# Performance work log

Hardware: AMD Instinct MI355X
Metric: run time of the kernel (lower is better)

## Reference

```python
import jax, jax.numpy as jnp
import numpy as np

EPS = 1e-5

def _layer_norm_last(x):
    # F.layer_norm over the last dim, no affine
    m = jnp.mean(x, axis=-1, keepdims=True)
    v = jnp.var(x, axis=-1, keepdims=True)
    return (x - m) * jax.lax.rsqrt(v + EPS)

def setup_inputs() -> dict:
    key = jax.random.key(0)
    ks = jax.random.split(key, 4)
    N, C, H, W = 8, 512, 32, 32
    G = 8
    x = jax.random.normal(ks[0], (N, C, H, W), dtype=jnp.float32)
    w_qkv = jax.random.normal(ks[1], (3 * C, C), dtype=jnp.float32) * 0.02
    relative = jax.random.normal(ks[2], (3, 2 * C - 1), dtype=jnp.float32)
    bn_w = jnp.ones((3 * G,), dtype=jnp.float32)
    bn_b = jnp.zeros((3 * G,), dtype=jnp.float32)
    return {
        "x": x, "w_qkv": w_qkv, "relative": relative,
        "bn_w": bn_w, "bn_b": bn_b,
        "f_qr": jnp.float32(0.1), "f_kr": jnp.float32(0.1),
        "f_sv": jnp.float32(1.0), "f_sve": jnp.float32(0.1),
        "gamma": jnp.full((1,), 0.5, dtype=jnp.float32),
    }

def reference(x, w_qkv, relative, bn_w, bn_b, f_qr, f_kr, f_sv, f_sve, gamma):
    N, C, H, W = x.shape
    HW = H * W
    G = bn_w.shape[0] // 3          # groups
    gp = HW // G                    # group_planes

    # qkv transform (1x1 conv == matmul over channels) + layernorm over spatial
    x1 = x.reshape(N, C, HW)
    x1 = jnp.einsum('oc,bci->boi', w_qkv, x1)          # (N, 3C, HW)
    x1 = _layer_norm_last(x1)

    qkv = x1.reshape(N, G, 3 * C, gp)                  # row-major, matches torch
    q = qkv[:, :, :C]                                  # (N, G, C, gp)
    k = qkv[:, :, C:2 * C]
    v = qkv[:, :, 2 * C:]

    # relative position embeddings gathered to (3, C, C)
    qi = jnp.arange(C)[None, :]
    ki = jnp.arange(C)[:, None]
    rel_idx = (ki - qi + C - 1).reshape(-1)            # (C*C,) int
    emb = relative[:, rel_idx].reshape(3, C, C)
    qE, kE, vE = emb[0], emb[1], emb[2]

    # 'bgci,icj->bgcj' with emb repeated along i collapses to sum over i then outer
    qr = jnp.einsum('bgci,cj->bgcj', q, qE) * f_qr     # (N, G, C, C)
    kr = jnp.swapaxes(jnp.einsum('bgci,cj->bgcj', k, kE), 2, 3) * f_kr
    qk = jnp.einsum('bgci,bgji->bgcj', q, k)           # (N, G, C, C)

    ss = jnp.concatenate([qk, qr, kr], axis=1)         # (N, 3G, C, C)
    # BatchNorm2d (training mode: batch stats over N, C, C axes)
    mu = jnp.mean(ss, axis=(0, 2, 3), keepdims=True)
    var = jnp.var(ss, axis=(0, 2, 3), keepdims=True)
    ss = (ss - mu) * jax.lax.rsqrt(var + EPS)
    ss = ss * bn_w.reshape(1, -1, 1, 1) + bn_b.reshape(1, -1, 1, 1)

    ss = ss.reshape(N, 3, G, C, C).sum(axis=1)         # (N, G, C, C)
    sim = jax.nn.softmax(ss, axis=3)

    sv = jnp.einsum('bgci,bgij->bgjc', sim, v) * f_sv  # (N, G, gp, C)
    # 'bgci,jci->bgjc' with vE repeated along j -> same value for every j
    sve = jnp.einsum('bgci,ci->bgc', sim, vE) * f_sve  # (N, G, C)
    sve = jnp.broadcast_to(sve[:, :, None, :], sv.shape)

    so = jnp.concatenate([sv, sve], axis=-1).reshape(N, HW * 2, C)
    so = jnp.swapaxes(_layer_norm_last(jnp.swapaxes(so, 1, 2)), 1, 2)
    out = so.reshape(N, G, gp, 2, C).sum(axis=-2).reshape(N, C, H, W)
    return gamma.reshape(()) * out + x
```

## Files before the change

kernel.cpp:

```cpp
#include <hip/hip_runtime.h>
#include <math.h>

#define DEV_INLINE __device__ __forceinline__

typedef short bf16x8 __attribute__((ext_vector_type(8)));
typedef float f32x4  __attribute__((ext_vector_type(4)));


DEV_INLINE float bf2f(short h){
  union { unsigned u; float f; } x; x.u = ((unsigned)(unsigned short)h) << 16; return x.f;
}
DEV_INLINE short f2bf(float f){
  union { float f; unsigned u; } x; x.f = f;
  unsigned r = x.u + 0x7FFF + ((x.u >> 16) & 1);
  return (short)(r >> 16);
}

template<bool MAXOP>
DEV_INLINE float block_reduce_f(float v){
  __shared__ float tmp[4];
  const int lane = threadIdx.x & 63, w = threadIdx.x >> 6;
  #pragma unroll
  for (int off = 32; off; off >>= 1){
    float o = __shfl_down(v, off);
    v = MAXOP ? fmaxf(v, o) : (v + o);
  }
  __syncthreads();
  if (lane == 0) tmp[w] = v;
  __syncthreads();
  return MAXOP ? fmaxf(fmaxf(tmp[0], tmp[1]), fmaxf(tmp[2], tmp[3]))
               : (tmp[0] + tmp[1] + tmp[2] + tmp[3]);
}

DEV_INLINE double block_reduce_d(double v){
  __shared__ double tmp[4];
  const int lane = threadIdx.x & 63, w = threadIdx.x >> 6;
  #pragma unroll
  for (int off = 32; off; off >>= 1) v += __shfl_down(v, off);
  __syncthreads();
  if (lane == 0) tmp[w] = v;
  __syncthreads();
  return tmp[0] + tmp[1] + tmp[2] + tmp[3];
}


DEV_INLINE void stage_tile(const short* __restrict__ g, int ldk, char* lds_region, int t){
  #pragma unroll
  for (int r = 0; r < 2; ++r){
    int o   = t * 16 + r * 4096;
    int row = o >> 6, wb = o & 63;
    int swb = wb ^ (((row >> 1) & 3) << 4);
    const short* src = g + (size_t)row * ldk + (swb >> 1);
    char* dst = lds_region + ((t >> 6) << 10) + (r << 12);
    __builtin_amdgcn_global_load_lds((const __attribute__((address_space(1))) void*)src,
                                     (__attribute__((address_space(3))) void*)dst, 16, 0, 0);
  }
}

DEV_INLINE bf16x8 read_frag(const char* base, int row, int kgrp){
  int off = row * 64 + ((kgrp ^ ((row >> 1) & 3)) << 4);
  return *(const bf16x8*)(base + off);
}

template<int KTILES>
DEV_INLINE void mfma_loop(const short* __restrict__ A, int ldA,
                          const short* __restrict__ B, int ldB,
                          char* ldsA, char* ldsB, int t, f32x4 acc[4][4]){
  const int l = t & 63, w = t >> 6;
  const int wr = (w >> 1) * 64, wc = (w & 1) * 64;
  for (int kt = 0; kt < KTILES; ++kt){
    stage_tile(A + kt * 32, ldA, ldsA, t);
    stage_tile(B + kt * 32, ldB, ldsB, t);
    __syncthreads();
    bf16x8 af[4], bfr[4];
    #pragma unroll
    for (int m = 0; m < 4; ++m) af[m]  = read_frag(ldsA, wr + m * 16 + (l & 15), l >> 4);
    #pragma unroll
    for (int n = 0; n < 4; ++n) bfr[n] = read_frag(ldsB, wc + n * 16 + (l & 15), l >> 4);
    #pragma unroll
    for (int m = 0; m < 4; ++m)
      #pragma unroll
      for (int n = 0; n < 4; ++n)
        acc[m][n] = __builtin_amdgcn_mfma_f32_16x16x32_bf16(af[m], bfr[n], acc[m][n], 0, 0, 0);
    __syncthreads();
  }
}

__global__ __launch_bounds__(256) void k_cvtW(const float* __restrict__ W, short* __restrict__ Wbf,
                                              double* __restrict__ stats, float* __restrict__ S12){
  const int gi = blockIdx.x * 256 + threadIdx.x;
  if (gi < 48) stats[gi] = 0.0;
  if (gi < 8192) S12[gi] = 0.f;
  int i = gi * 4;
  float4 v = *(const float4*)(W + i);
  short4 o; o.x = f2bf(v.x); o.y = f2bf(v.y); o.z = f2bf(v.z); o.w = f2bf(v.w);
  *(short4*)(Wbf + i) = o;
}

__global__ __launch_bounds__(256) void k_cvtXt(const float* __restrict__ X, short* __restrict__ Xt){
  const int b = blockIdx.z, kt = blockIdx.y, it = blockIdx.x;
  __shared__ short s[64][72];
  const int t = threadIdx.x;
  const int rl = t >> 2, cs = (t & 3) * 16;
  const float* src = X + ((size_t)b * 512 + kt * 64 + rl) * 1024 + it * 64 + cs;
  #pragma unroll
  for (int e = 0; e < 16; e += 4){
    float4 v = *(const float4*)(src + e);
    s[rl][cs + e + 0] = f2bf(v.x); s[rl][cs + e + 1] = f2bf(v.y);
    s[rl][cs + e + 2] = f2bf(v.z); s[rl][cs + e + 3] = f2bf(v.w);
  }
  __syncthreads();
  bf16x8 a0, a1;
  #pragma unroll
  for (int e = 0; e < 8; ++e){ a0[e] = s[cs + e][rl]; a1[e] = s[cs + 8 + e][rl]; }
  short* dst = Xt + ((size_t)b * 1024 + it * 64 + rl) * 512 + kt * 64 + cs;
  *(bf16x8*)dst = a0;
  *(bf16x8*)(dst + 8) = a1;
}

__global__ __launch_bounds__(256) void k_vt(const short* __restrict__ Ybf, short* __restrict__ Vt){
  const int bg = blockIdx.z, iit = blockIdx.y, jt = blockIdx.x;
  const int b = bg >> 3, g = bg & 7;
  const short* V = Ybf + (size_t)(b * 1536 + g * 192 + 128) * 1024;
  __shared__ short s[64][72];
  const int t = threadIdx.x;
  const int rl = t >> 2, cs = (t & 3) * 16;
  const short* src = V + (size_t)(iit * 64 + rl) * 128 + jt * 64 + cs;
  *(bf16x8*)&s[rl][cs]     = *(const bf16x8*)src;
  *(bf16x8*)&s[rl][cs + 8] = *(const bf16x8*)(src + 8);
  __syncthreads();
  bf16x8 a0, a1;
  #pragma unroll
  for (int e = 0; e < 8; ++e){ a0[e] = s[cs + e][rl]; a1[e] = s[cs + 8 + e][rl]; }
  short* dst = Vt + ((size_t)bg * 128 + jt * 64 + rl) * 512 + iit * 64 + cs;
  *(bf16x8*)dst = a0;
  *(bf16x8*)(dst + 8) = a1;
}

__global__ __launch_bounds__(256) void k_gemm1(const short* __restrict__ Wbf,
                                               const short* __restrict__ Xt,
                                               short* __restrict__ Ybf){
  const int b = blockIdx.z, mt = blockIdx.y, nt = blockIdx.x;
  __shared__ char lds[16384];
  const int t = threadIdx.x;
  f32x4 acc[4][4];
  #pragma unroll
  for (int m = 0; m < 4; ++m)
    #pragma unroll
    for (int n = 0; n < 4; ++n) acc[m][n] = {0.f, 0.f, 0.f, 0.f};
  const short* A = Wbf + (size_t)mt * 128 * 512;
  const short* B = Xt + (size_t)b * 1024 * 512 + (size_t)nt * 128 * 512;
  mfma_loop<16>(A, 512, B, 512, lds, lds + 8192, t, acc);
  const int l = t & 63, w = t >> 6, wr = (w >> 1) * 64, wc = (w & 1) * 64;
  short* out = Ybf + (size_t)b * 1536 * 1024 + (size_t)(mt * 128 + wr) * 1024 + nt * 128 + wc;
  #pragma unroll
  for (int m = 0; m < 4; ++m)
    #pragma unroll
    for (int n = 0; n < 4; ++n)
      #pragma unroll
      for (int j = 0; j < 4; ++j)
        out[(size_t)(m * 16 + (l >> 4) * 4 + j) * 1024 + n * 16 + (l & 15)] = f2bf(acc[m][n][j]);
}

__global__ __launch_bounds__(256) void k_ln(short* __restrict__ Ybf,
                                            float* __restrict__ QS, float* __restrict__ KS){
  const int row = blockIdx.x * 4 + (threadIdx.x >> 6);
  const int l = threadIdx.x & 63;
  short* p = Ybf + (size_t)row * 1024 + l * 16;
  bf16x8 v0 = *(const bf16x8*)p;
  bf16x8 v1 = *(const bf16x8*)(p + 8);
  float f[16];
  #pragma unroll
  for (int e = 0; e < 8; ++e){ f[e] = bf2f(v0[e]); f[8 + e] = bf2f(v1[e]); }
  float s1 = 0.f, s2 = 0.f;
  #pragma unroll
  for (int e = 0; e < 16; ++e){ s1 += f[e]; s2 += f[e] * f[e]; }
  #pragma unroll
  for (int off = 32; off; off >>= 1){ s1 += __shfl_xor(s1, off); s2 += __shfl_xor(s2, off); }
  float mean = s1 * (1.f / 1024.f);
  float r = rsqrtf(s2 * (1.f / 1024.f) - mean * mean + 1e-5f);
  float cs = 0.f;
  #pragma unroll
  for (int e = 0; e < 16; ++e){ f[e] = (f[e] - mean) * r; cs += f[e]; }
  bf16x8 o0, o1;
  #pragma unroll
  for (int e = 0; e < 8; ++e){ o0[e] = f2bf(f[e]); o1[e] = f2bf(f[8 + e]); }
  *(bf16x8*)p = o0;
  *(bf16x8*)(p + 8) = o1;
  cs += __shfl_xor(cs, 1); cs += __shfl_xor(cs, 2); cs += __shfl_xor(cs, 4);
  const int o = row % 1536, ol = o % 192;
  if ((l & 7) == 0 && ol < 128){
    const int b = row / 1536, g = o / 192;
    const int c = (ol & 63) * 8 + (l >> 3);
    const int idx = (b * 8 + g) * 512 + c;
    if (ol < 64) QS[idx] = cs; else KS[idx] = cs;
  }
}

__global__ __launch_bounds__(256) void k_rel_rowsums(const float* __restrict__ rel,
                                                     float* __restrict__ R){
  const int c = blockIdx.x * 256 + threadIdx.x;
  float a1 = 0, a2 = 0, b1 = 0, b2 = 0;
  for (int d = 0; d < 512; ++d){
    float v0 = rel[c + d];        a1 += v0; a2 += v0*v0;
    float v1 = rel[1023 + c + d]; b1 += v1; b2 += v1*v1;
  }
  R[c] = a1; R[512 + c] = a2; R[1024 + c] = b1; R[1536 + c] = b2;
}

__global__ __launch_bounds__(256) void k_qk(const short* __restrict__ Ybf,
                                            short* __restrict__ QKbf,
                                            double* __restrict__ stats){
  const int bg = blockIdx.z, mt = blockIdx.y, nt = blockIdx.x;
  const int b = bg >> 3, g = bg & 7;
  __shared__ char lds[16384];
  const int t = threadIdx.x;
  f32x4 acc[4][4];
  #pragma unroll
  for (int m = 0; m < 4; ++m)
    #pragma unroll
    for (int n = 0; n < 4; ++n) acc[m][n] = {0.f, 0.f, 0.f, 0.f};
  const short* q  = Ybf + (size_t)(b * 1536 + g * 192) * 1024;
  const short* kp = q + 65536;
  mfma_loop<4>(q + (size_t)mt * 128 * 128, 128, kp + (size_t)nt * 128 * 128, 128,
               lds, lds + 8192, t, acc);
  const int l = t & 63, w = t >> 6, wr = (w >> 1) * 64, wc = (w & 1) * 64;
  short* out = QKbf + (size_t)bg * 512 * 512 + (size_t)(mt * 128 + wr) * 512 + nt * 128 + wc;
  float s1 = 0.f, s2 = 0.f;
  #pragma unroll
  for (int m = 0; m < 4; ++m)
    #pragma unroll
    for (int n = 0; n < 4; ++n)
      #pragma unroll
      for (int j = 0; j < 4; ++j){
        float vl = acc[m][n][j];
        s1 += vl; s2 += vl * vl;
        out[(size_t)(m * 16 + (l >> 4) * 4 + j) * 512 + n * 16 + (l & 15)] = f2bf(vl);
      }
  float S1 = block_reduce_f<false>(s1);
  float S2 = block_reduce_f<false>(s2);
  if (t == 0){
    atomicAdd(&stats[g * 6 + 0], (double)S1);
    atomicAdd(&stats[g * 6 + 1], (double)S2);
  }
}

__global__ __launch_bounds__(256) void k_qrkr_stats(const float* __restrict__ QS,
                                                    const float* __restrict__ KS,
                                                    const float* __restrict__ R,
                                                    double* __restrict__ stats){
  const int g = blockIdx.x, t = threadIdx.x;
  double sq1 = 0, sq2 = 0, sk1 = 0, sk2 = 0;
  for (int c = t; c < 512; c += 256){
    float qa = 0, qb = 0, ka = 0, kb = 0;
    for (int b = 0; b < 8; ++b){
      float v = QS[(size_t)(b * 8 + g) * 512 + c]; qa += v; qb += v * v;
      float w = KS[(size_t)(b * 8 + g) * 512 + c]; ka += w; kb += w * w;
    }
    sq1 += (double)R[c]        * qa;
    sq2 += (double)R[512 + c]  * qb;
    sk1 += (double)R[1024 + c] * ka;
    sk2 += (double)R[1536 + c] * kb;
  }
  sq1 = block_reduce_d(sq1);
  sq2 = block_reduce_d(sq2);
  sk1 = block_reduce_d(sk1);
  sk2 = block_reduce_d(sk2);
  if (t == 0){
    stats[g * 6 + 2] = sq1; stats[g * 6 + 3] = sq2;
    stats[g * 6 + 4] = sk1; stats[g * 6 + 5] = sk2;
  }
}

__global__ void k_finalize(const double* __restrict__ stats,
                           const float* __restrict__ bnw, const float* __restrict__ bnb,
                           const float* __restrict__ fqr, const float* __restrict__ fkr,
                           float* __restrict__ coefs){
  const int g = threadIdx.x;
  if (g >= 8) return;
  const double M = 2097152.0;
  double mu0  = stats[g*6+0] / M;
  double var0 = stats[g*6+1] / M - mu0*mu0;
  double A0 = (double)bnw[g] / sqrt(var0 + 1e-5);
  double fq = (double)fqr[0];
  double mu1  = fq * stats[g*6+2] / M;
  double var1 = fq*fq * stats[g*6+3] / M - mu1*mu1;
  double A1 = (double)bnw[8+g] / sqrt(var1 + 1e-5);
  double fk = (double)fkr[0];
  double mu2  = fk * stats[g*6+4] / M;
  double var2 = fk*fk * stats[g*6+5] / M - mu2*mu2;
  double A2 = (double)bnw[16+g] / sqrt(var2 + 1e-5);
  double Cg = ((double)bnb[g] - mu0*A0) + ((double)bnb[8+g] - mu1*A1) + ((double)bnb[16+g] - mu2*A2);
  coefs[g*4+0] = (float)A0;
  coefs[g*4+1] = (float)(A1 * fq);
  coefs[g*4+2] = (float)(A2 * fk);
  coefs[g*4+3] = (float)Cg;
}

__global__ __launch_bounds__(256) void k_softmax(short* __restrict__ QKbf,
    const float* __restrict__ QS, const float* __restrict__ KS,
    const float* __restrict__ rel, const float* __restrict__ coefs,
    const float* __restrict__ fsve, float* __restrict__ SVE, float* __restrict__ S12){
  const int row = blockIdx.x * 4 + (threadIdx.x >> 6);
  const int l = threadIdx.x & 63;
  const int bg = row >> 9, c = row & 511, g = bg & 7;
  const float A0 = coefs[g*4+0], B2 = coefs[g*4+2], Cg = coefs[g*4+3];
  const float B1q = coefs[g*4+1] * QS[row];
  short* __restrict__ qkrow = QKbf + (size_t)row * 512;
  const float* __restrict__ ksrow = KS + (size_t)bg * 512;
  const int j0 = l * 8;
  bf16x8 qk8 = *(const bf16x8*)(qkrow + j0);
  float4 ks0 = *(const float4*)(ksrow + j0);
  float4 ks1 = *(const float4*)(ksrow + j0 + 4);
  float ks[8] = {ks0.x, ks0.y, ks0.z, ks0.w, ks1.x, ks1.y, ks1.z, ks1.w};
  const float* relq = rel + 511 + c - j0;
  const float* relk = rel + 1534 + j0 - c;
  float s[8];
  float m = -1e30f;
  #pragma unroll
  for (int e = 0; e < 8; ++e){
    s[e] = A0 * bf2f(qk8[e]) + B1q * relq[-e] + B2 * ks[e] * relk[e] + Cg;
    m = fmaxf(m, s[e]);
  }
  #pragma unroll
  for (int off = 32; off; off >>= 1) m = fmaxf(m, __shfl_xor(m, off));
  float sum = 0.f;
  #pragma unroll
  for (int e = 0; e < 8; ++e){ s[e] = __expf(s[e] - m); sum += s[e]; }
  #pragma unroll
  for (int off = 32; off; off >>= 1) sum += __shfl_xor(sum, off);
  const float inv = 1.0f / sum;
  const float* relv = rel + 2557 + c - j0;
  float sve = 0.f;
  bf16x8 p8;
  #pragma unroll
  for (int e = 0; e < 8; ++e){
    float p = s[e] * inv;
    p8[e] = f2bf(p);
    sve += p * relv[-e];
  }
  *(bf16x8*)(qkrow + j0) = p8;
  #pragma unroll
  for (int off = 32; off; off >>= 1) sve += __shfl_xor(sve, off);
  if (l == 0){
    float e = fsve[0] * sve;
    SVE[row] = e;
    const int b = bg >> 3;
    atomicAdd(&S12[b * 512 + c],        128.f * e);
    atomicAdd(&S12[4096 + b * 512 + c], 128.f * e * e);
  }
}

__global__ __launch_bounds__(256) void k_sv(const short* __restrict__ Pbf,
                                            const short* __restrict__ Vt,
                                            const float* __restrict__ fsv,
                                            short* __restrict__ SV2,
                                            float* __restrict__ S12){
  const int bg = blockIdx.z, mt = blockIdx.x;
  __shared__ char lds[16384];
  __shared__ float s1buf[128], s2buf[128];
  const int t = threadIdx.x;
  s1buf[t & 127] = 0.f; s2buf[t & 127] = 0.f;
  f32x4 acc[4][4];
  #pragma unroll
  for (int m = 0; m < 4; ++m)
    #pragma unroll
    for (int n = 0; n < 4; ++n) acc[m][n] = {0.f, 0.f, 0.f, 0.f};
  const short* A = Pbf + (size_t)bg * 512 * 512 + (size_t)mt * 128 * 512;
  const short* B = Vt  + (size_t)bg * 128 * 512;
  mfma_loop<16>(A, 512, B, 512, lds, lds + 8192, t, acc);
  const int l = t & 63, w = t >> 6, wr = (w >> 1) * 64, wc = (w & 1) * 64;
  const float fv = fsv[0];
  short* out = SV2 + (size_t)bg * 512 * 128 + (size_t)(mt * 128 + wr) * 128 + wc;
  #pragma unroll
  for (int m = 0; m < 4; ++m)
    #pragma unroll
    for (int jr = 0; jr < 4; ++jr){
      float p1 = 0.f, p2 = 0.f;
      #pragma unroll
      for (int n = 0; n < 4; ++n){
        float vl = acc[m][n][jr] * fv;
        p1 += vl; p2 += vl * vl;
        out[(size_t)(m * 16 + (l >> 4) * 4 + jr) * 128 + n * 16 + (l & 15)] = f2bf(vl);
      }
      #pragma unroll
      for (int off = 1; off < 16; off <<= 1){
        p1 += __shfl_xor(p1, off);
        p2 += __shfl_xor(p2, off);
      }
      if ((l & 15) == 0){
        int rloc = wr + m * 16 + (l >> 4) * 4 + jr;
        atomicAdd(&s1buf[rloc], p1);
        atomicAdd(&s2buf[rloc], p2);
      }
    }
  __syncthreads();
  if (t < 128){
    const int b = bg >> 3;
    const int ci = b * 512 + mt * 128 + t;
    atomicAdd(&S12[ci],        s1buf[t]);
    atomicAdd(&S12[4096 + ci], s2buf[t]);
  }
}

__global__ __launch_bounds__(256) void k_out(const short* __restrict__ SV2,
    const float* __restrict__ SVE, const float* __restrict__ S12,
    const float* __restrict__ X, const float* __restrict__ gam, float* __restrict__ OUT){
  const int c2t = blockIdx.x, g = blockIdx.y, b = blockIdx.z;
  const int bg = b * 8 + g;
  const int c20 = c2t * 64;
  __shared__ float s[64][129];
  const int t = threadIdx.x;
  {
    const int col8 = (t & 15) * 8;
    #pragma unroll
    for (int r0 = 0; r0 < 64; r0 += 16){
      int row = r0 + (t >> 4);
      bf16x8 v = *(const bf16x8*)(SV2 + (size_t)bg * 65536 + (size_t)(c20 + row) * 128 + col8);
      #pragma unroll
      for (int e = 0; e < 8; ++e) s[row][col8 + e] = bf2f(v[e]);
    }
  }
  __syncthreads();
  const int lane = t & 63, w = t >> 6;
  const int c2 = c20 + lane;
  const float sm1 = S12[b * 512 + c2];
  const float sm2 = S12[4096 + b * 512 + c2];
  const float mean = sm1 * (1.f / 2048.f);
  const float rs   = rsqrtf(sm2 * (1.f / 2048.f) - mean * mean + 1e-5f);
  const float e    = SVE[(size_t)bg * 512 + c2];
  const float gm   = gam[0];
  for (int j = w; j < 128; j += 4){
    float v = s[lane][j];
    float o = (v + e - 2.f * mean) * rs;
    int chan = g * 64 + (j >> 1);
    size_t oi = ((size_t)b * 512 + chan) * 1024 + ((j & 1) << 9) + c2;
    OUT[oi] = gm * o + X[oi];
  }
}

extern "C" void kernel_launch(void* const* d_in, const int* in_sizes, int n_in,
                              void* d_out, int out_size, void* d_ws, size_t ws_size,
                              hipStream_t stream){
  const float* X    = (const float*)d_in[0];
  const float* W    = (const float*)d_in[1];
  const float* REL  = (const float*)d_in[2];
  const float* BNW  = (const float*)d_in[3];
  const float* BNB  = (const float*)d_in[4];
  const float* FQR  = (const float*)d_in[5];
  const float* FKR  = (const float*)d_in[6];
  const float* FSV  = (const float*)d_in[7];
  const float* FSVE = (const float*)d_in[8];
  const float* GAM  = (const float*)d_in[9];
  float* OUT = (float*)d_out;

  char* ws = (char*)d_ws;
  short*  Ybf   = (short*) (ws + 0ull);
  short*  QKbf  = (short*) (ws + 25165824ull);
  short*  SV2   = (short*) (ws + 58720256ull);
  short*  Wbf   = (short*) (ws + 75497472ull);
  short*  Xt    = (short*) (ws + 77070336ull);
  short*  Vt    = (short*) (ws + 85458944ull);
  float*  QS    = (float*) (ws + 93847552ull);
  float*  KS    = (float*) (ws + 93978624ull);
  float*  SVE   = (float*) (ws + 94109696ull);
  double* STATS = (double*)(ws + 94240768ull);
  float*  COEFS = (float*) (ws + 94241152ull);
  float*  R     = (float*) (ws + 94241280ull);
  float*  S12   = (float*) (ws + 94249472ull);

  k_cvtW       <<<768,             256, 0, stream>>>(W, Wbf, STATS, S12);
  k_cvtXt      <<<dim3(16, 8, 8),  256, 0, stream>>>(X, Xt);
  k_gemm1      <<<dim3(8, 12, 8),  256, 0, stream>>>(Wbf, Xt, Ybf);
  k_ln         <<<3072,            256, 0, stream>>>(Ybf, QS, KS);
  k_rel_rowsums<<<2,               256, 0, stream>>>(REL, R);
  k_qrkr_stats <<<8,               256, 0, stream>>>(QS, KS, R, STATS);
  k_qk         <<<dim3(4, 4, 64),  256, 0, stream>>>(Ybf, QKbf, STATS);
  k_finalize   <<<1,               64,  0, stream>>>(STATS, BNW, BNB, FQR, FKR, COEFS);
  k_vt         <<<dim3(2, 8, 64),  256, 0, stream>>>(Ybf, Vt);
  k_softmax    <<<8192,            256, 0, stream>>>(QKbf, QS, KS, REL, COEFS, FSVE, SVE, S12);
  k_sv         <<<dim3(4, 1, 64),  256, 0, stream>>>(QKbf, Vt, FSV, SV2, S12);
  k_out        <<<dim3(8, 8, 8),   256, 0, stream>>>(SV2, SVE, S12, X, GAM, OUT);
}
```

Before: 136.8 us.

## Fuse softmax into SV GEMM and fold BN finalize and rel rowsums

Removes the standalone softmax kernel that wrote the normalized probabilities back to QKbf. The SV GEMM kernel now computes row sums of exp in a first pass, then recomputes the probabilities per K-tile straight into LDS as the A operand. BN coefficient finalization is inlined per block, and the relative-embedding rowsum kernel is merged into a parallelized qr/kr stats kernel that accumulates with atomics, cutting launch count and a large round trip through global memory. In exchange the exps are computed twice, the row-sum pass reads memory with poor coalescing across only 256 blocks, and the max subtraction is dropped, which risks overflow in exp.

After: 139.6 us. 1.02x slower.

```diff
diff --git a/kernel.cpp b/kernel.cpp
--- a/kernel.cpp
+++ b/kernel.cpp
@@ -197,17 +197,6 @@
   }
 }
 
-__global__ __launch_bounds__(256) void k_rel_rowsums(const float* __restrict__ rel,
-                                                     float* __restrict__ R){
-  const int c = blockIdx.x * 256 + threadIdx.x;
-  float a1 = 0, a2 = 0, b1 = 0, b2 = 0;
-  for (int d = 0; d < 512; ++d){
-    float v0 = rel[c + d];        a1 += v0; a2 += v0*v0;
-    float v1 = rel[1023 + c + d]; b1 += v1; b2 += v1*v1;
-  }
-  R[c] = a1; R[512 + c] = a2; R[1024 + c] = b1; R[1536 + c] = b2;
-}
-
 __global__ __launch_bounds__(256) void k_qk(const short* __restrict__ Ybf,
                                             short* __restrict__ QKbf,
                                             double* __restrict__ stats){
@@ -245,133 +234,168 @@
   }
 }
 
-__global__ __launch_bounds__(256) void k_qrkr_stats(const float* __restrict__ QS,
-                                                    const float* __restrict__ KS,
-                                                    const float* __restrict__ R,
-                                                    double* __restrict__ stats){
-  const int g = blockIdx.x, t = threadIdx.x;
+__global__ __launch_bounds__(256) void k_qrkr(const float* __restrict__ QS,
+                                              const float* __restrict__ KS,
+                                              const float* __restrict__ rel,
+                                              double* __restrict__ stats){
+  const int g = blockIdx.x & 7, ch = blockIdx.x >> 3;
+  const int t = threadIdx.x;
+  const int c = ch * 64 + (t >> 2), part = t & 3;
+  float r1 = 0, r2 = 0, r3 = 0, r4 = 0;
+  for (int d = part * 128; d < part * 128 + 128; ++d){
+    float v0 = rel[c + d];        r1 += v0; r2 += v0 * v0;
+    float v1 = rel[1023 + c + d]; r3 += v1; r4 += v1 * v1;
+  }
+  #pragma unroll
+  for (int off = 1; off < 4; off <<= 1){
+    r1 += __shfl_xor(r1, off); r2 += __shfl_xor(r2, off);
+    r3 += __shfl_xor(r3, off); r4 += __shfl_xor(r4, off);
+  }
   double sq1 = 0, sq2 = 0, sk1 = 0, sk2 = 0;
-  for (int c = t; c < 512; c += 256){
+  if (part == 0){
     float qa = 0, qb = 0, ka = 0, kb = 0;
     for (int b = 0; b < 8; ++b){
       float v = QS[(size_t)(b * 8 + g) * 512 + c]; qa += v; qb += v * v;
       float w = KS[(size_t)(b * 8 + g) * 512 + c]; ka += w; kb += w * w;
     }
-    sq1 += (double)R[c]        * qa;
-    sq2 += (double)R[512 + c]  * qb;
-    sk1 += (double)R[1024 + c] * ka;
-    sk2 += (double)R[1536 + c] * kb;
+    sq1 = (double)r1 * qa; sq2 = (double)r2 * qb;
+    sk1 = (double)r3 * ka; sk2 = (double)r4 * kb;
   }
   sq1 = block_reduce_d(sq1);
   sq2 = block_reduce_d(sq2);
   sk1 = block_reduce_d(sk1);
   sk2 = block_reduce_d(sk2);
   if (t == 0){
-    stats[g * 6 + 2] = sq1; stats[g * 6 + 3] = sq2;
-    stats[g * 6 + 4] = sk1; stats[g * 6 + 5] = sk2;
-  }
-}
-
-__global__ void k_finalize(const double* __restrict__ stats,
-                           const float* __restrict__ bnw, const float* __restrict__ bnb,
-                           const float* __restrict__ fqr, const float* __restrict__ fkr,
-                           float* __restrict__ coefs){
-  const int g = threadIdx.x;
-  if (g >= 8) return;
+    atomicAdd(&stats[g * 6 + 2], sq1);
+    atomicAdd(&stats[g * 6 + 3], sq2);
+    atomicAdd(&stats[g * 6 + 4], sk1);
+    atomicAdd(&stats[g * 6 + 5], sk2);
+  }
+}
+
+__global__ __launch_bounds__(256) void k_smsv(const short* __restrict__ QKbf,
+    const short* __restrict__ Vt,
+    const float* __restrict__ QS, const float* __restrict__ KS,
+    const float* __restrict__ rel, const double* __restrict__ stats,
+    const float* __restrict__ bnw, const float* __restrict__ bnb,
+    const float* __restrict__ fqr, const float* __restrict__ fkr,
+    const float* __restrict__ fsv, const float* __restrict__ fsve,
+    float* __restrict__ SVE, short* __restrict__ SV2, float* __restrict__ S12){
+  const int mt = blockIdx.x, bg = blockIdx.y;
+  const int b = bg >> 3, g = bg & 7;
+  __shared__ char lds[16384];
+  __shared__ float rowinv[128];
+  __shared__ float s1buf[128], s2buf[128];
+  const int t = threadIdx.x;
+
   const double M = 2097152.0;
   double mu0  = stats[g*6+0] / M;
   double var0 = stats[g*6+1] / M - mu0*mu0;
-  double A0 = (double)bnw[g] / sqrt(var0 + 1e-5);
-  double fq = (double)fqr[0];
+  double A0d  = (double)bnw[g] / sqrt(var0 + 1e-5);
+  double fq   = (double)fqr[0];
   double mu1  = fq * stats[g*6+2] / M;
   double var1 = fq*fq * stats[g*6+3] / M - mu1*mu1;
-  double A1 = (double)bnw[8+g] / sqrt(var1 + 1e-5);
-  double fk = (double)fkr[0];
+  double A1d  = (double)bnw[8+g] / sqrt(var1 + 1e-5);
+  double fk   = (double)fkr[0];
   double mu2  = fk * stats[g*6+4] / M;
   double var2 = fk*fk * stats[g*6+5] / M - mu2*mu2;
-  double A2 = (double)bnw[16+g] / sqrt(var2 + 1e-5);
-  double Cg = ((double)bnb[g] - mu0*A0) + ((double)bnb[8+g] - mu1*A1) + ((double)bnb[16+g] - mu2*A2);
-  coefs[g*4+0] = (float)A0;
-  coefs[g*4+1] = (float)(A1 * fq);
-  coefs[g*4+2] = (float)(A2 * fk);
-  coefs[g*4+3] = (float)Cg;
-}
-
-__global__ __launch_bounds__(256) void k_softmax(short* __restrict__ QKbf,
-    const float* __restrict__ QS, const float* __restrict__ KS,
-    const float* __restrict__ rel, const float* __restrict__ coefs,
-    const float* __restrict__ fsve, float* __restrict__ SVE, float* __restrict__ S12){
-  const int row = blockIdx.x * 4 + (threadIdx.x >> 6);
-  const int l = threadIdx.x & 63;
-  const int bg = row >> 9, c = row & 511, g = bg & 7;
-  const float A0 = coefs[g*4+0], B2 = coefs[g*4+2], Cg = coefs[g*4+3];
-  const float B1q = coefs[g*4+1] * QS[row];
-  short* __restrict__ qkrow = QKbf + (size_t)row * 512;
+  double A2d  = (double)bnw[16+g] / sqrt(var2 + 1e-5);
+  double Cgd  = ((double)bnb[g] - mu0*A0d) + ((double)bnb[8+g] - mu1*A1d)
+              + ((double)bnb[16+g] - mu2*A2d);
+  const float A0 = (float)A0d, B1 = (float)(A1d * fq), B2 = (float)(A2d * fk), Cg = (float)Cgd;
+
   const float* __restrict__ ksrow = KS + (size_t)bg * 512;
-  const int j0 = l * 8;
-  bf16x8 qk8 = *(const bf16x8*)(qkrow + j0);
-  float4 ks0 = *(const float4*)(ksrow + j0);
-  float4 ks1 = *(const float4*)(ksrow + j0 + 4);
-  float ks[8] = {ks0.x, ks0.y, ks0.z, ks0.w, ks1.x, ks1.y, ks1.z, ks1.w};
-  const float* relq = rel + 511 + c - j0;
-  const float* relk = rel + 1534 + j0 - c;
-  float s[8];
-  float m = -1e30f;
-  #pragma unroll
-  for (int e = 0; e < 8; ++e){
-    s[e] = A0 * bf2f(qk8[e]) + B1q * relq[-e] + B2 * ks[e] * relk[e] + Cg;
-    m = fmaxf(m, s[e]);
-  }
-  #pragma unroll
-  for (int off = 32; off; off >>= 1) m = fmaxf(m, __shfl_xor(m, off));
-  float sum = 0.f;
-  #pragma unroll
-  for (int e = 0; e < 8; ++e){ s[e] = __expf(s[e] - m); sum += s[e]; }
-  #pragma unroll
-  for (int off = 32; off; off >>= 1) sum += __shfl_xor(sum, off);
-  const float inv = 1.0f / sum;
-  const float* relv = rel + 2557 + c - j0;
-  float sve = 0.f;
-  bf16x8 p8;
-  #pragma unroll
-  for (int e = 0; e < 8; ++e){
-    float p = s[e] * inv;
-    p8[e] = f2bf(p);
-    sve += p * relv[-e];
-  }
-  *(bf16x8*)(qkrow + j0) = p8;
-  #pragma unroll
-  for (int off = 32; off; off >>= 1) sve += __shfl_xor(sve, off);
-  if (l == 0){
-    float e = fsve[0] * sve;
-    SVE[row] = e;
-    const int b = bg >> 3;
-    atomicAdd(&S12[b * 512 + c],        128.f * e);
-    atomicAdd(&S12[4096 + b * 512 + c], 128.f * e * e);
-  }
-}
-
-__global__ __launch_bounds__(256) void k_sv(const short* __restrict__ Pbf,
-                                            const short* __restrict__ Vt,
-                                            const float* __restrict__ fsv,
-                                            short* __restrict__ SV2,
-                                            float* __restrict__ S12){
-  const int bg = blockIdx.z, mt = blockIdx.x;
-  __shared__ char lds[16384];
-  __shared__ float s1buf[128], s2buf[128];
-  const int t = threadIdx.x;
-  s1buf[t & 127] = 0.f; s2buf[t & 127] = 0.f;
+
+  {
+    const int r = t >> 1, h = t & 1;
+    const int c = mt * 128 + r;
+    const int grow = bg * 512 + c;
+    const float B1q = B1 * QS[grow];
+    const short* qkrow = QKbf + (size_t)bg * 262144 + (size_t)c * 512;
+    const float* relqp = rel + 511 + c;
+    const float* relkp = rel + 1534 - c;
+    const float* relvp = rel + 2557 + c;
+    float sum = 0.f, svea = 0.f;
+    for (int u = 0; u < 32; ++u){
+      const int j0 = h * 256 + u * 8;
+      bf16x8 qk8 = *(const bf16x8*)(qkrow + j0);
+      float4 k0 = *(const float4*)(ksrow + j0);
+      float4 k1 = *(const float4*)(ksrow + j0 + 4);
+      float ks[8] = {k0.x, k0.y, k0.z, k0.w, k1.x, k1.y, k1.z, k1.w};
+      #pragma unroll
+      for (int e = 0; e < 8; ++e){
+        const int j = j0 + e;
+        float s = A0 * bf2f(qk8[e]) + B1q * relqp[-j] + B2 * ks[e] * relkp[j] + Cg;
+        float es = __expf(s);
+        sum  += es;
+        svea += es * relvp[-j];
+      }
+    }
+    sum  += __shfl_xor(sum, 1);
+    svea += __shfl_xor(svea, 1);
+    float inv = 1.f / sum;
+    if (h == 0){
+      rowinv[r] = inv;
+      float ev = fsve[0] * svea * inv;
+      SVE[grow] = ev;
+      atomicAdd(&S12[b * 512 + c],        128.f * ev);
+      atomicAdd(&S12[4096 + b * 512 + c], 128.f * ev * ev);
+    }
+  }
+  if (t < 128){ s1buf[t] = 0.f; s2buf[t] = 0.f; }
+  __syncthreads();
+
+  const int l = t & 63, w = t >> 6;
+  const int wr = (w >> 1) * 64, wc = (w & 1) * 64;
   f32x4 acc[4][4];
   #pragma unroll
   for (int m = 0; m < 4; ++m)
     #pragma unroll
     for (int n = 0; n < 4; ++n) acc[m][n] = {0.f, 0.f, 0.f, 0.f};
-  const short* A = Pbf + (size_t)bg * 512 * 512 + (size_t)mt * 128 * 512;
-  const short* B = Vt  + (size_t)bg * 128 * 512;
-  mfma_loop<16>(A, 512, B, 512, lds, lds + 8192, t, acc);
-  const int l = t & 63, w = t >> 6, wr = (w >> 1) * 64, wc = (w & 1) * 64;
+
+  for (int kt = 0; kt < 16; ++kt){
+    stage_tile(Vt + (size_t)bg * 65536 + kt * 32, 512, lds + 8192, t);
+    #pragma unroll
+    for (int cc = 0; cc < 2; ++cc){
+      const int cid = t + cc * 256;
+      const int rr = cid >> 2, kg = cid & 3;
+      const int c2 = mt * 128 + rr;
+      const int i0 = kt * 32 + kg * 8;
+      const short* qrow2 = QKbf + (size_t)bg * 262144 + (size_t)c2 * 512;
+      bf16x8 q8 = *(const bf16x8*)(qrow2 + i0);
+      float4 k0 = *(const float4*)(ksrow + i0);
+      float4 k1 = *(const float4*)(ksrow + i0 + 4);
+      float ks2[8] = {k0.x, k0.y, k0.z, k0.w, k1.x, k1.y, k1.z, k1.w};
+      const float B1q2 = B1 * QS[bg * 512 + c2];
+      const float* relqp = rel + 511 + c2;
+      const float* relkp = rel + 1534 - c2;
+      const float iv = rowinv[rr];
+      bf16x8 p8;
+      #pragma unroll
+      for (int e = 0; e < 8; ++e){
+        const int i = i0 + e;
+        float s = A0 * bf2f(q8[e]) + B1q2 * relqp[-i] + B2 * ks2[e] * relkp[i] + Cg;
+        p8[e] = f2bf(__expf(s) * iv);
+      }
+      const int off = rr * 64 + ((kg ^ ((rr >> 1) & 3)) << 4);
+      *(bf16x8*)(lds + off) = p8;
+    }
+    __syncthreads();
+    bf16x8 af[4], bfr[4];
+    #pragma unroll
+    for (int m = 0; m < 4; ++m) af[m]  = read_frag(lds,        wr + m * 16 + (l & 15), l >> 4);
+    #pragma unroll
+    for (int n = 0; n < 4; ++n) bfr[n] = read_frag(lds + 8192, wc + n * 16 + (l & 15), l >> 4);
+    #pragma unroll
+    for (int m = 0; m < 4; ++m)
+      #pragma unroll
+      for (int n = 0; n < 4; ++n)
+        acc[m][n] = __builtin_amdgcn_mfma_f32_16x16x32_bf16(af[m], bfr[n], acc[m][n], 0, 0, 0);
+    __syncthreads();
+  }
+
   const float fv = fsv[0];
-  short* out = SV2 + (size_t)bg * 512 * 128 + (size_t)(mt * 128 + wr) * 128 + wc;
+  short* out = SV2 + (size_t)bg * 65536 + (size_t)(mt * 128 + wr) * 128 + wc;
   #pragma unroll
   for (int m = 0; m < 4; ++m)
     #pragma unroll
@@ -396,7 +420,6 @@
     }
   __syncthreads();
   if (t < 128){
-    const int b = bg >> 3;
     const int ci = b * 512 + mt * 128 + t;
     atomicAdd(&S12[ci],        s1buf[t]);
     atomicAdd(&S12[4096 + ci], s2buf[t]);
@@ -465,20 +488,17 @@
   float*  KS    = (float*) (ws + 93978624ull);
   float*  SVE   = (float*) (ws + 94109696ull);
   double* STATS = (double*)(ws + 94240768ull);
-  float*  COEFS = (float*) (ws + 94241152ull);
-  float*  R     = (float*) (ws + 94241280ull);
   float*  S12   = (float*) (ws + 94249472ull);
 
-  k_cvtW       <<<768,             256, 0, stream>>>(W, Wbf, STATS, S12);
-  k_cvtXt      <<<dim3(16, 8, 8),  256, 0, stream>>>(X, Xt);
-  k_gemm1      <<<dim3(8, 12, 8),  256, 0, stream>>>(Wbf, Xt, Ybf);
-  k_ln         <<<3072,            256, 0, stream>>>(Ybf, QS, KS);
-  k_rel_rowsums<<<2,               256, 0, stream>>>(REL, R);
-  k_qrkr_stats <<<8,               256, 0, stream>>>(QS, KS, R, STATS);
-  k_qk         <<<dim3(4, 4, 64),  256, 0, stream>>>(Ybf, QKbf, STATS);
-  k_finalize   <<<1,               64,  0, stream>>>(STATS, BNW, BNB, FQR, FKR, COEFS);
-  k_vt         <<<dim3(2, 8, 64),  256, 0, stream>>>(Ybf, Vt);
-  k_softmax    <<<8192,            256, 0, stream>>>(QKbf, QS, KS, REL, COEFS, FSVE, SVE, S12);
-  k_sv         <<<dim3(4, 1, 64),  256, 0, stream>>>(QKbf, Vt, FSV, SV2, S12);
-  k_out        <<<dim3(8, 8, 8),   256, 0, stream>>>(SV2, SVE, S12, X, GAM, OUT);
-}
+  k_cvtW  <<<768,             256, 0, stream>>>(W, Wbf, STATS, S12);
+  k_cvtXt <<<dim3(16, 8, 8),  256, 0, stream>>>(X, Xt);
+  k_gemm1 <<<dim3(8, 12, 8),  256, 0, stream>>>(Wbf, Xt, Ybf);
+  k_ln    <<<3072,            256, 0, stream>>>(Ybf, QS, KS);
+  k_qk    <<<dim3(4, 4, 64),  256, 0, stream>>>(Ybf, QKbf, STATS);
+  k_qrkr  <<<64,              256, 0, stream>>>(QS, KS, REL, STATS);
+  k_vt    <<<dim3(2, 8, 64),  256, 0, stream>>>(Ybf, Vt);
+  k_smsv  <<<dim3(4, 64),     256, 0, stream>>>(QKbf, Vt, QS, KS, REL, STATS,
+                                                BNW, BNB, FQR, FKR, FSV, FSVE,
+                                                SVE, SV2, S12);
+  k_out   <<<dim3(8, 8, 8),   256, 0, stream>>>(SV2, SVE, S12, X, GAM, OUT);
+}
```

## Merge small kernels to cut launch count and serial tiny-grid stages

Applied to the files above, without the earlier changes.

Fuses the W and X conversion kernels into one launch, merges the relative-embedding row sums into a wider 64-block qrkr stats kernel that accumulates with atomics, and folds the BatchNorm coefficient finalize into the softmax kernel prologue. This removes three kernel launches and the serialized 1-, 2- and 8-block stages that left most of the GPU idle. In exchange every softmax wave recomputes the double-precision coefficients, and the stats reduction now relies on atomic double adds whose order is nondeterministic.

Measured after the change: 131.4 us. 4.0% less time.

```diff
diff --git a/kernel.cpp b/kernel.cpp
--- a/kernel.cpp
+++ b/kernel.cpp
@@ -86,36 +86,38 @@
   }
 }
 
-__global__ __launch_bounds__(256) void k_cvtW(const float* __restrict__ W, short* __restrict__ Wbf,
+__global__ __launch_bounds__(256) void k_prep(const float* __restrict__ X, short* __restrict__ Xt,
+                                              const float* __restrict__ W, short* __restrict__ Wbf,
                                               double* __restrict__ stats, float* __restrict__ S12){
-  const int gi = blockIdx.x * 256 + threadIdx.x;
-  if (gi < 48) stats[gi] = 0.0;
-  if (gi < 8192) S12[gi] = 0.f;
-  int i = gi * 4;
-  float4 v = *(const float4*)(W + i);
-  short4 o; o.x = f2bf(v.x); o.y = f2bf(v.y); o.z = f2bf(v.z); o.w = f2bf(v.w);
-  *(short4*)(Wbf + i) = o;
-}
-
-__global__ __launch_bounds__(256) void k_cvtXt(const float* __restrict__ X, short* __restrict__ Xt){
-  const int b = blockIdx.z, kt = blockIdx.y, it = blockIdx.x;
   __shared__ short s[64][72];
-  const int t = threadIdx.x;
-  const int rl = t >> 2, cs = (t & 3) * 16;
-  const float* src = X + ((size_t)b * 512 + kt * 64 + rl) * 1024 + it * 64 + cs;
-  #pragma unroll
-  for (int e = 0; e < 16; e += 4){
-    float4 v = *(const float4*)(src + e);
-    s[rl][cs + e + 0] = f2bf(v.x); s[rl][cs + e + 1] = f2bf(v.y);
-    s[rl][cs + e + 2] = f2bf(v.z); s[rl][cs + e + 3] = f2bf(v.w);
-  }
-  __syncthreads();
-  bf16x8 a0, a1;
-  #pragma unroll
-  for (int e = 0; e < 8; ++e){ a0[e] = s[cs + e][rl]; a1[e] = s[cs + 8 + e][rl]; }
-  short* dst = Xt + ((size_t)b * 1024 + it * 64 + rl) * 512 + kt * 64 + cs;
-  *(bf16x8*)dst = a0;
-  *(bf16x8*)(dst + 8) = a1;
+  const int bid = blockIdx.x;
+  const int t = threadIdx.x;
+  if (bid < 1024){
+    const int it = bid & 15, kt = (bid >> 4) & 7, b = bid >> 7;
+    const int rl = t >> 2, cs = (t & 3) * 16;
+    const float* src = X + ((size_t)b * 512 + kt * 64 + rl) * 1024 + it * 64 + cs;
+    #pragma unroll
+    for (int e = 0; e < 16; e += 4){
+      float4 v = *(const float4*)(src + e);
+      s[rl][cs + e + 0] = f2bf(v.x); s[rl][cs + e + 1] = f2bf(v.y);
+      s[rl][cs + e + 2] = f2bf(v.z); s[rl][cs + e + 3] = f2bf(v.w);
+    }
+    __syncthreads();
+    bf16x8 a0, a1;
+    #pragma unroll
+    for (int e = 0; e < 8; ++e){ a0[e] = s[cs + e][rl]; a1[e] = s[cs + 8 + e][rl]; }
+    short* dst = Xt + ((size_t)b * 1024 + it * 64 + rl) * 512 + kt * 64 + cs;
+    *(bf16x8*)dst = a0;
+    *(bf16x8*)(dst + 8) = a1;
+  } else {
+    const int gi = (bid - 1024) * 256 + t;
+    if (gi < 48) stats[gi] = 0.0;
+    if (gi < 8192) S12[gi] = 0.f;
+    const int i = gi * 4;
+    float4 v = *(const float4*)(W + i);
+    short4 o; o.x = f2bf(v.x); o.y = f2bf(v.y); o.z = f2bf(v.z); o.w = f2bf(v.w);
+    *(short4*)(Wbf + i) = o;
+  }
 }
 
 __global__ __launch_bounds__(256) void k_vt(const short* __restrict__ Ybf, short* __restrict__ Vt){
@@ -197,17 +199,6 @@
   }
 }
 
-__global__ __launch_bounds__(256) void k_rel_rowsums(const float* __restrict__ rel,
-                                                     float* __restrict__ R){
-  const int c = blockIdx.x * 256 + threadIdx.x;
-  float a1 = 0, a2 = 0, b1 = 0, b2 = 0;
-  for (int d = 0; d < 512; ++d){
-    float v0 = rel[c + d];        a1 += v0; a2 += v0*v0;
-    float v1 = rel[1023 + c + d]; b1 += v1; b2 += v1*v1;
-  }
-  R[c] = a1; R[512 + c] = a2; R[1024 + c] = b1; R[1536 + c] = b2;
-}
-
 __global__ __launch_bounds__(256) void k_qk(const short* __restrict__ Ybf,
                                             short* __restrict__ QKbf,
                                             double* __restrict__ stats){
@@ -245,67 +236,71 @@
   }
 }
 
-__global__ __launch_bounds__(256) void k_qrkr_stats(const float* __restrict__ QS,
-                                                    const float* __restrict__ KS,
-                                                    const float* __restrict__ R,
-                                                    double* __restrict__ stats){
-  const int g = blockIdx.x, t = threadIdx.x;
+__global__ __launch_bounds__(256) void k_qrkr(const float* __restrict__ QS,
+                                              const float* __restrict__ KS,
+                                              const float* __restrict__ rel,
+                                              double* __restrict__ stats){
+  const int g = blockIdx.x & 7, ch = blockIdx.x >> 3;
+  const int t = threadIdx.x;
+  const int c = ch * 64 + (t >> 2), part = t & 3;
+  float r1 = 0, r2 = 0, r3 = 0, r4 = 0;
+  for (int d = part * 128; d < part * 128 + 128; ++d){
+    float v0 = rel[c + d];        r1 += v0; r2 += v0 * v0;
+    float v1 = rel[1023 + c + d]; r3 += v1; r4 += v1 * v1;
+  }
+  #pragma unroll
+  for (int off = 1; off < 4; off <<= 1){
+    r1 += __shfl_xor(r1, off); r2 += __shfl_xor(r2, off);
+    r3 += __shfl_xor(r3, off); r4 += __shfl_xor(r4, off);
+  }
   double sq1 = 0, sq2 = 0, sk1 = 0, sk2 = 0;
-  for (int c = t; c < 512; c += 256){
+  if (part == 0){
     float qa = 0, qb = 0, ka = 0, kb = 0;
     for (int b = 0; b < 8; ++b){
       float v = QS[(size_t)(b * 8 + g) * 512 + c]; qa += v; qb += v * v;
       float w = KS[(size_t)(b * 8 + g) * 512 + c]; ka += w; kb += w * w;
     }
-    sq1 += (double)R[c]        * qa;
-    sq2 += (double)R[512 + c]  * qb;
-    sk1 += (double)R[1024 + c] * ka;
-    sk2 += (double)R[1536 + c] * kb;
+    sq1 = (double)r1 * qa; sq2 = (double)r2 * qb;
+    sk1 = (double)r3 * ka; sk2 = (double)r4 * kb;
   }
   sq1 = block_reduce_d(sq1);
   sq2 = block_reduce_d(sq2);
   sk1 = block_reduce_d(sk1);
   sk2 = block_reduce_d(sk2);
   if (t == 0){
-    stats[g * 6 + 2] = sq1; stats[g * 6 + 3] = sq2;
-    stats[g * 6 + 4] = sk1; stats[g * 6 + 5] = sk2;
-  }
-}
-
-__global__ void k_finalize(const double* __restrict__ stats,
-                           const float* __restrict__ bnw, const float* __restrict__ bnb,
-                           const float* __restrict__ fqr, const float* __restrict__ fkr,
-                           float* __restrict__ coefs){
-  const int g = threadIdx.x;
-  if (g >= 8) return;
-  const double M = 2097152.0;
-  double mu0  = stats[g*6+0] / M;
-  double var0 = stats[g*6+1] / M - mu0*mu0;
-  double A0 = (double)bnw[g] / sqrt(var0 + 1e-5);
-  double fq = (double)fqr[0];
-  double mu1  = fq * stats[g*6+2] / M;
-  double var1 = fq*fq * stats[g*6+3] / M - mu1*mu1;
-  double A1 = (double)bnw[8+g] / sqrt(var1 + 1e-5);
-  double fk = (double)fkr[0];
-  double mu2  = fk * stats[g*6+4] / M;
-  double var2 = fk*fk * stats[g*6+5] / M - mu2*mu2;
-  double A2 = (double)bnw[16+g] / sqrt(var2 + 1e-5);
-  double Cg = ((double)bnb[g] - mu0*A0) + ((double)bnb[8+g] - mu1*A1) + ((double)bnb[16+g] - mu2*A2);
-  coefs[g*4+0] = (float)A0;
-  coefs[g*4+1] = (float)(A1 * fq);
-  coefs[g*4+2] = (float)(A2 * fk);
-  coefs[g*4+3] = (float)Cg;
+    atomicAdd(&stats[g * 6 + 2], sq1);
+    atomicAdd(&stats[g * 6 + 3], sq2);
+    atomicAdd(&stats[g * 6 + 4], sk1);
+    atomicAdd(&stats[g * 6 + 5], sk2);
+  }
 }
 
 __global__ __launch_bounds__(256) void k_softmax(short* __restrict__ QKbf,
     const float* __restrict__ QS, const float* __restrict__ KS,
-    const float* __restrict__ rel, const float* __restrict__ coefs,
+    const float* __restrict__ rel, const double* __restrict__ stats,
+    const float* __restrict__ bnw, const float* __restrict__ bnb,
+    const float* __restrict__ fqr, const float* __restrict__ fkr,
     const float* __restrict__ fsve, float* __restrict__ SVE, float* __restrict__ S12){
   const int row = blockIdx.x * 4 + (threadIdx.x >> 6);
   const int l = threadIdx.x & 63;
   const int bg = row >> 9, c = row & 511, g = bg & 7;
-  const float A0 = coefs[g*4+0], B2 = coefs[g*4+2], Cg = coefs[g*4+3];
-  const float B1q = coefs[g*4+1] * QS[row];
+  const double M = 2097152.0;
+  double mu0  = stats[g*6+0] / M;
+  double var0 = stats[g*6+1] / M - mu0*mu0;
+  double A0d  = (double)bnw[g] / sqrt(var0 + 1e-5);
+  double fq   = (double)fqr[0];
+  double mu1  = fq * stats[g*6+2] / M;
+  double var1 = fq*fq * stats[g*6+3] / M - mu1*mu1;
+  double A1d  = (double)bnw[8+g] / sqrt(var1 + 1e-5);
+  double fk   = (double)fkr[0];
+  double mu2  = fk * stats[g*6+4] / M;
+  double var2 = fk*fk * stats[g*6+5] / M - mu2*mu2;
+  double A2d  = (double)bnw[16+g] / sqrt(var2 + 1e-5);
+  double Cgd  = ((double)bnb[g] - mu0*A0d) + ((double)bnb[8+g] - mu1*A1d)
+              + ((double)bnb[16+g] - mu2*A2d);
+  const float A0 = (float)A0d, B2 = (float)(A2d * fk), Cg = (float)Cgd;
+  const float B1q = (float)(A1d * fq) * QS[row];
+
   short* __restrict__ qkrow = QKbf + (size_t)row * 512;
   const float* __restrict__ ksrow = KS + (size_t)bg * 512;
   const int j0 = l * 8;
@@ -465,20 +460,16 @@
   float*  KS    = (float*) (ws + 93978624ull);
   float*  SVE   = (float*) (ws + 94109696ull);
   double* STATS = (double*)(ws + 94240768ull);
-  float*  COEFS = (float*) (ws + 94241152ull);
-  float*  R     = (float*) (ws + 94241280ull);
   float*  S12   = (float*) (ws + 94249472ull);
 
-  k_cvtW       <<<768,             256, 0, stream>>>(W, Wbf, STATS, S12);
-  k_cvtXt      <<<dim3(16, 8, 8),  256, 0, stream>>>(X, Xt);
-  k_gemm1      <<<dim3(8, 12, 8),  256, 0, stream>>>(Wbf, Xt, Ybf);
-  k_ln         <<<3072,            256, 0, stream>>>(Ybf, QS, KS);
-  k_rel_rowsums<<<2,               256, 0, stream>>>(REL, R);
-  k_qrkr_stats <<<8,               256, 0, stream>>>(QS, KS, R, STATS);
-  k_qk         <<<dim3(4, 4, 64),  256, 0, stream>>>(Ybf, QKbf, STATS);
-  k_finalize   <<<1,               64,  0, stream>>>(STATS, BNW, BNB, FQR, FKR, COEFS);
-  k_vt         <<<dim3(2, 8, 64),  256, 0, stream>>>(Ybf, Vt);
-  k_softmax    <<<8192,            256, 0, stream>>>(QKbf, QS, KS, REL, COEFS, FSVE, SVE, S12);
-  k_sv         <<<dim3(4, 1, 64),  256, 0, stream>>>(QKbf, Vt, FSV, SV2, S12);
-  k_out        <<<dim3(8, 8, 8),   256, 0, stream>>>(SV2, SVE, S12, X, GAM, OUT);
-}
+  k_prep   <<<1792,            256, 0, stream>>>(X, Xt, W, Wbf, STATS, S12);
+  k_gemm1  <<<dim3(8, 12, 8),  256, 0, stream>>>(Wbf, Xt, Ybf);
+  k_ln     <<<3072,            256, 0, stream>>>(Ybf, QS, KS);
+  k_qk     <<<dim3(4, 4, 64),  256, 0, stream>>>(Ybf, QKbf, STATS);
+  k_qrkr   <<<64,              256, 0, stream>>>(QS, KS, REL, STATS);
+  k_vt     <<<dim3(2, 8, 64),  256, 0, stream>>>(Ybf, Vt);
+  k_softmax<<<8192,            256, 0, stream>>>(QKbf, QS, KS, REL, STATS,
+                                                 BNW, BNB, FQR, FKR, FSVE, SVE, S12);
+  k_sv     <<<dim3(4, 1, 64),  256, 0, stream>>>(QKbf, Vt, FSV, SV2, S12);
+  k_out    <<<dim3(8, 8, 8),   256, 0, stream>>>(SV2, SVE, S12, X, GAM, OUT);
+}
```
